# Performance work log

Hardware: AMD Instinct MI355X
Metric: run time of the kernel (lower is better)

The kernel has to match this reference:

```python
import jax, jax.numpy as jnp
import numpy as np

B, N, C, H = 4, 1024, 768, 12
HD = C // H

def setup_inputs() -> dict:
    key = jax.random.key(0)
    ks = jax.random.split(key, 6)
    s = 0.02
    return {
        "x": jax.random.normal(ks[0], (B, N, C), jnp.float32),
        "attn_bias": jax.random.normal(ks[1], (H, N, N), jnp.float32),
        "qkv_w": jax.random.normal(ks[2], (C, 3 * C), jnp.float32) * s,
        "qkv_b": jax.random.normal(ks[3], (3 * C,), jnp.float32) * s,
        "proj_w": jax.random.normal(ks[4], (C, C), jnp.float32) * s,
        "proj_b": jax.random.normal(ks[5], (C,), jnp.float32) * s,
    }

def reference(x, attn_bias, qkv_w, qkv_b, proj_w, proj_b):
    b, n, c = x.shape
    scale = HD ** -0.5
    qkv = x @ qkv_w + qkv_b                      # [B,N,3C]
    qkv = qkv.reshape(b, n, 3, H, HD)
    q = qkv[:, :, 0].transpose(0, 2, 1, 3)       # [B,H,N,HD]
    k = qkv[:, :, 1].transpose(0, 2, 1, 3)
    v = qkv[:, :, 2].transpose(0, 2, 1, 3)
    attn = jnp.einsum('bhqd,bhkd->bhqk', q, k) * scale
    attn = attn + attn_bias[None]                # broadcast over batch
    attn = jax.nn.softmax(attn, axis=-1)
    y = jnp.einsum('bhqk,bhkd->bhqd', attn, v)   # [B,H,N,HD]
    y = y.transpose(0, 2, 1, 3).reshape(b, n, c)
    return y @ proj_w + proj_b
```

## Files before the change

### kernel.cpp

```cpp
#include <hip/hip_runtime.h>
#include <hip/hip_bf16.h>

constexpr int BATCH = 4;
constexpr int NSEQ  = 1024;
constexpr int CDIM  = 768;
constexpr int NHEAD = 12;
constexpr int HDIM  = 64;
constexpr int MTOT  = BATCH * NSEQ;
constexpr int QKVN  = 3 * CDIM;

typedef __bf16 bf16x8 __attribute__((ext_vector_type(8)));
typedef float  f32x4  __attribute__((ext_vector_type(4)));

__device__ __forceinline__ unsigned short f2bf(float f) {
    unsigned u = __builtin_bit_cast(unsigned, f);
    unsigned r = u + 0x7FFFu + ((u >> 16) & 1u);
    return (unsigned short)(r >> 16);
}

#define GLOAD_LDS16(gp, lp)                                                    \
    __builtin_amdgcn_global_load_lds(                                          \
        (const __attribute__((address_space(1))) void*)(gp),                   \
        (__attribute__((address_space(3))) void*)(lp), 16, 0, 0)

__global__ __launch_bounds__(256) void cvt_f32_bf16(
    const float* __restrict__ in, unsigned short* __restrict__ out, int n4)
{
    int i = blockIdx.x * 256 + threadIdx.x;
    if (i < n4) {
        float4 a = reinterpret_cast<const float4*>(in)[i];
        ushort4 h;
        h.x = f2bf(a.x); h.y = f2bf(a.y); h.z = f2bf(a.z); h.w = f2bf(a.w);
        reinterpret_cast<ushort4*>(out)[i] = h;
    }
}

__global__ __launch_bounds__(256) void tcvt_f32_bf16(
    const float* __restrict__ in, unsigned short* __restrict__ out, int R, int C)
{
    __shared__ unsigned short t[32][33];
    const int c0 = blockIdx.x * 32, r0 = blockIdx.y * 32;
    const int tc = threadIdx.x & 31, tr = threadIdx.x >> 5;
    #pragma unroll
    for (int i = 0; i < 4; i++)
        t[tc][tr + 8 * i] = f2bf(in[(size_t)(r0 + tr + 8 * i) * C + c0 + tc]);
    __syncthreads();
    #pragma unroll
    for (int i = 0; i < 4; i++)
        out[(size_t)(c0 + tr + 8 * i) * R + r0 + tc] = t[tr + 8 * i][tc];
}

__global__ __launch_bounds__(256) void qkv_gemm(
    const unsigned short* __restrict__ xb,
    const unsigned short* __restrict__ wt,
    const float* __restrict__ bias,
    unsigned short* __restrict__ qbuf, unsigned short* __restrict__ kbuf,
    unsigned short* __restrict__ vtbuf)
{
    __shared__ unsigned short As[128 * 32];
    __shared__ unsigned short Bs[128 * 32];
    const int tid  = threadIdx.x;
    const int lane = tid & 63;
    const int wid  = tid >> 6;
    const int wm = (wid >> 1) * 64, wn = (wid & 1) * 64;
    const int g = lane >> 4, li = lane & 15;
    const int m0 = blockIdx.y * 128;
    const int n0 = blockIdx.x * 128;
    const int srow = lane >> 2;
    const int scol = (lane & 3) * 8;

    f32x4 acc[4][4];
    #pragma unroll
    for (int i = 0; i < 4; i++)
        #pragma unroll
        for (int j = 0; j < 4; j++) acc[i][j] = f32x4{0.f, 0.f, 0.f, 0.f};

    for (int k0 = 0; k0 < CDIM; k0 += 32) {
        __syncthreads();
        #pragma unroll
        for (int c = 0; c < 2; c++) {
            int row = wid * 32 + c * 16 + srow;
            GLOAD_LDS16(&xb[(size_t)(m0 + row) * CDIM + k0 + scol],
                        &As[(wid * 32 + c * 16) * 32]);
            GLOAD_LDS16(&wt[(size_t)(n0 + row) * CDIM + k0 + scol],
                        &Bs[(wid * 32 + c * 16) * 32]);
        }
        __syncthreads();
        bf16x8 a[4], b[4];
        #pragma unroll
        for (int mt = 0; mt < 4; mt++)
            a[mt] = *reinterpret_cast<const bf16x8*>(&As[(wm + 16 * mt + li) * 32 + 8 * g]);
        #pragma unroll
        for (int nt = 0; nt < 4; nt++)
            b[nt] = *reinterpret_cast<const bf16x8*>(&Bs[(wn + 16 * nt + li) * 32 + 8 * g]);
        #pragma unroll
        for (int mt = 0; mt < 4; mt++)
            #pragma unroll
            for (int nt = 0; nt < 4; nt++)
                acc[mt][nt] = __builtin_amdgcn_mfma_f32_16x16x32_bf16(a[mt], b[nt], acc[mt][nt], 0, 0, 0);
    }

    #pragma unroll
    for (int mt = 0; mt < 4; mt++) {
        #pragma unroll
        for (int nt = 0; nt < 4; nt++) {
            int col  = n0 + wn + 16 * nt + li;
            int tsel = col / CDIM;
            int rem  = col - tsel * CDIM;
            int h_ = rem >> 6, d = rem & 63;
            float bv = bias[col];
            float sc = (tsel == 0) ? 0.125f : 1.0f;
            #pragma unroll
            for (int r = 0; r < 4; r++) {
                int m  = m0 + wm + 16 * mt + 4 * g + r;
                int b_ = m >> 10, s = m & 1023;
                unsigned short hv = f2bf((acc[mt][nt][r] + bv) * sc);
                if (tsel == 0)
                    qbuf[(((size_t)b_ * NHEAD + h_) * NSEQ + s) * HDIM + d] = hv;
                else if (tsel == 1)
                    kbuf[(((size_t)b_ * NHEAD + h_) * NSEQ + s) * HDIM + d] = hv;
                else
                    vtbuf[(((size_t)b_ * NHEAD + h_) * HDIM + d) * NSEQ + s] = hv;
            }
        }
    }
}

__global__ __launch_bounds__(256, 3) void attn_kernel(
    const unsigned short* __restrict__ qbuf,
    const unsigned short* __restrict__ kbuf,
    const unsigned short* __restrict__ vtbuf,
    const float* __restrict__ bias,
    unsigned short* __restrict__ ybuf)
{
    __shared__ unsigned short Kl[2][64 * 64];
    __shared__ unsigned short Vl[2][64 * 64];
    __shared__ unsigned short Ps[4][16][72];

    const int tid  = threadIdx.x;
    const int lane = tid & 63;
    const int wid  = tid >> 6;
    const int g = lane >> 4, li = lane & 15;
    const int srow8 = lane >> 3;
    const int scs   = (lane & 7) ^ srow8;
    const int bh = blockIdx.y;
    const int b_ = bh / NHEAD, h_ = bh % NHEAD;
    const int qw = blockIdx.x * 64 + wid * 16;

    const unsigned short* qb = qbuf + (size_t)bh * NSEQ * HDIM;
    const unsigned short* kb = kbuf + (size_t)bh * NSEQ * HDIM;
    const unsigned short* vb = vtbuf + (size_t)bh * HDIM * NSEQ;
    const float* bb = bias + (size_t)h_ * NSEQ * NSEQ;

#define STAGE_KV(T, KL, VL)                                                    \
    {                                                                          \
        _Pragma("unroll") for (int i = 0; i < 2; i++) {                        \
            GLOAD_LDS16(kb + (size_t)((T) * 64 + wid * 16 + i * 8 + srow8) * HDIM + scs * 8, \
                        (KL) + (wid * 16 + i * 8) * 64);                       \
            GLOAD_LDS16(vb + (size_t)(wid * 16 + i * 8 + srow8) * NSEQ + (T) * 64 + scs * 8, \
                        (VL) + (wid * 16 + i * 8) * 64);                       \
        }                                                                      \
    }

#define COMPUTE_TILE(KS, VS, T)                                                \
    {                                                                          \
        float bv[4][4];                                                        \
        _Pragma("unroll") for (int kt = 0; kt < 4; kt++)                       \
            _Pragma("unroll") for (int r = 0; r < 4; r++)                      \
                bv[kt][r] = bb[(size_t)(qw + 4 * g + r) * NSEQ + (T) * 64 + 16 * kt + li]; \
        f32x4 sacc[4];                                                         \
        _Pragma("unroll") for (int kt = 0; kt < 4; kt++)                       \
            sacc[kt] = f32x4{0.f, 0.f, 0.f, 0.f};                              \
        _Pragma("unroll") for (int kt = 0; kt < 4; kt++)                       \
            _Pragma("unroll") for (int dd = 0; dd < 2; dd++) {                 \
                bf16x8 kf = *reinterpret_cast<const bf16x8*>(                  \
                    (KS) + (16 * kt + li) * 64 + (((4 * dd + g) ^ (li & 7)) * 8)); \
                sacc[kt] = __builtin_amdgcn_mfma_f32_16x16x32_bf16(qf[dd], kf, sacc[kt], 0, 0, 0); \
            }                                                                  \
        _Pragma("unroll") for (int kt = 0; kt < 4; kt++)                       \
            _Pragma("unroll") for (int r = 0; r < 4; r++) {                    \
                float pv = __expf(sacc[kt][r] + bv[kt][r]);                    \
                lpart[r] += pv;                                                \
                Ps[wid][4 * g + r][16 * kt + li] = f2bf(pv);                   \
            }                                                                  \
        _Pragma("unroll") for (int kk = 0; kk < 2; kk++) {                     \
            bf16x8 pf = *reinterpret_cast<const bf16x8*>(&Ps[wid][li][32 * kk + 8 * g]); \
            _Pragma("unroll") for (int dt = 0; dt < 4; dt++) {                 \
                bf16x8 vf = *reinterpret_cast<const bf16x8*>(                  \
                    (VS) + (16 * dt + li) * 64 + (((4 * kk + g) ^ (li & 7)) * 8)); \
                oacc[dt] = __builtin_amdgcn_mfma_f32_16x16x32_bf16(pf, vf, oacc[dt], 0, 0, 0); \
            }                                                                  \
        }                                                                      \
    }

    bf16x8 qf[2];
    #pragma unroll
    for (int dd = 0; dd < 2; dd++)
        qf[dd] = *reinterpret_cast<const bf16x8*>(&qb[(size_t)(qw + li) * HDIM + 32 * dd + 8 * g]);

    f32x4 oacc[4];
    #pragma unroll
    for (int dt = 0; dt < 4; dt++) oacc[dt] = f32x4{0.f, 0.f, 0.f, 0.f};
    float lpart[4] = {0.f, 0.f, 0.f, 0.f};

    STAGE_KV(0, Kl[0], Vl[0]);
    __syncthreads();

    for (int j = 0; j < 8; ++j) {
        const int tA = 2 * j;
        STAGE_KV(tA + 1, Kl[1], Vl[1]);
        COMPUTE_TILE(Kl[0], Vl[0], tA);
        __syncthreads();

        if (j < 7) STAGE_KV(tA + 2, Kl[0], Vl[0]);
        COMPUTE_TILE(Kl[1], Vl[1], tA + 1);
        __syncthreads();
    }

    float linv[4];
    #pragma unroll
    for (int r = 0; r < 4; r++) {
        float s = lpart[r];
        s += __shfl_xor(s, 1);
        s += __shfl_xor(s, 2);
        s += __shfl_xor(s, 4);
        s += __shfl_xor(s, 8);
        linv[r] = 1.f / s;
    }
    #pragma unroll
    for (int dt = 0; dt < 4; dt++)
        #pragma unroll
        for (int r = 0; r < 4; r++) {
            float o = oacc[dt][r] * linv[r];
            int sq = qw + 4 * g + r;
            ybuf[((size_t)b_ * NSEQ + sq) * CDIM + h_ * HDIM + 16 * dt + li] = f2bf(o);
        }
#undef STAGE_KV
#undef COMPUTE_TILE
}

__global__ __launch_bounds__(256) void proj_gemm(
    const unsigned short* __restrict__ yb,
    const unsigned short* __restrict__ pwt,
    const float* __restrict__ bias, float* __restrict__ out)
{
    __shared__ unsigned short As[128 * 32];
    __shared__ unsigned short Bs[128 * 32];
    const int tid  = threadIdx.x;
    const int lane = tid & 63;
    const int wid  = tid >> 6;
    const int wm = (wid >> 1) * 64, wn = (wid & 1) * 64;
    const int g = lane >> 4, li = lane & 15;
    const int m0 = blockIdx.y * 128;
    const int n0 = blockIdx.x * 128;
    const int srow = lane >> 2;
    const int scol = (lane & 3) * 8;

    f32x4 acc[4][4];
    #pragma unroll
    for (int i = 0; i < 4; i++)
        #pragma unroll
        for (int j = 0; j < 4; j++) acc[i][j] = f32x4{0.f, 0.f, 0.f, 0.f};

    for (int k0 = 0; k0 < CDIM; k0 += 32) {
        __syncthreads();
        #pragma unroll
        for (int c = 0; c < 2; c++) {
            int row = wid * 32 + c * 16 + srow;
            GLOAD_LDS16(&yb[(size_t)(m0 + row) * CDIM + k0 + scol],
                        &As[(wid * 32 + c * 16) * 32]);
            GLOAD_LDS16(&pwt[(size_t)(n0 + row) * CDIM + k0 + scol],
                        &Bs[(wid * 32 + c * 16) * 32]);
        }
        __syncthreads();
        bf16x8 a[4], b[4];
        #pragma unroll
        for (int mt = 0; mt < 4; mt++)
            a[mt] = *reinterpret_cast<const bf16x8*>(&As[(wm + 16 * mt + li) * 32 + 8 * g]);
        #pragma unroll
        for (int nt = 0; nt < 4; nt++)
            b[nt] = *reinterpret_cast<const bf16x8*>(&Bs[(wn + 16 * nt + li) * 32 + 8 * g]);
        #pragma unroll
        for (int mt = 0; mt < 4; mt++)
            #pragma unroll
            for (int nt = 0; nt < 4; nt++)
                acc[mt][nt] = __builtin_amdgcn_mfma_f32_16x16x32_bf16(a[mt], b[nt], acc[mt][nt], 0, 0, 0);
    }

    #pragma unroll
    for (int mt = 0; mt < 4; mt++)
        #pragma unroll
        for (int nt = 0; nt < 4; nt++) {
            int col = n0 + wn + 16 * nt + li;
            float bv = bias[col];
            #pragma unroll
            for (int r = 0; r < 4; r++) {
                int m = m0 + wm + 16 * mt + 4 * g + r;
                out[(size_t)m * CDIM + col] = acc[mt][nt][r] + bv;
            }
        }
}

extern "C" void kernel_launch(void* const* d_in, const int* in_sizes, int n_in,
                              void* d_out, int out_size, void* d_ws, size_t ws_size,
                              hipStream_t stream) {
    const float* x         = (const float*)d_in[0];
    const float* attn_bias = (const float*)d_in[1];
    const float* qkv_w     = (const float*)d_in[2];
    const float* qkv_b     = (const float*)d_in[3];
    const float* proj_w    = (const float*)d_in[4];
    const float* proj_b    = (const float*)d_in[5];
    float* out = (float*)d_out;

    const size_t per = (size_t)BATCH * NHEAD * NSEQ * HDIM;
    unsigned short* qbuf  = (unsigned short*)d_ws;
    unsigned short* kbuf  = qbuf + per;
    unsigned short* vtbuf = kbuf + per;
    unsigned short* xb    = vtbuf + per;
    unsigned short* qwt   = xb + per;
    unsigned short* pwt   = qwt + (size_t)QKVN * CDIM;
    unsigned short* ybuf  = xb;

    cvt_f32_bf16<<<(MTOT * CDIM / 4 + 255) / 256, 256, 0, stream>>>(
        x, xb, MTOT * CDIM / 4);
    tcvt_f32_bf16<<<dim3(QKVN / 32, CDIM / 32), 256, 0, stream>>>(
        qkv_w, qwt, CDIM, QKVN);
    tcvt_f32_bf16<<<dim3(CDIM / 32, CDIM / 32), 256, 0, stream>>>(
        proj_w, pwt, CDIM, CDIM);

    qkv_gemm<<<dim3(QKVN / 128, MTOT / 128), 256, 0, stream>>>(
        xb, qwt, qkv_b, qbuf, kbuf, vtbuf);
    attn_kernel<<<dim3(NSEQ / 64, BATCH * NHEAD), 256, 0, stream>>>(
        qbuf, kbuf, vtbuf, attn_bias, ybuf);
    proj_gemm<<<dim3(CDIM / 128, MTOT / 128), 256, 0, stream>>>(
        ybuf, pwt, proj_b, out);
}
```

Before: 106.8 us.

## Split attention over key halves, keep P in registers, add combine kernel

The attention kernel now splits the 1024 keys into two halves across a third grid dimension, writing unnormalised bf16 partial outputs and row sums that a new combine kernel merges and normalises. Scores are computed as K·Q so that exponentiated probabilities can be packed directly into MFMA operand registers, removing the LDS staging of P. The QKV GEMM permutes K rows within 32-row groups to match this layout, and the bias is loaded with vector loads. This raises block count and occupancy, at the cost of an extra kernel launch, extra workspace traffic, and a bf16 rounding of partial outputs.

Result: slower. 121.5 us (+13.7%).

```diff
diff --git a/kernel.cpp b/kernel.cpp
--- a/kernel.cpp
+++ b/kernel.cpp
@@ -8,6 +8,7 @@
 constexpr int HDIM  = 64;
 constexpr int MTOT  = BATCH * NSEQ;
 constexpr int QKVN  = 3 * CDIM;
+constexpr int NBH   = BATCH * NHEAD;
 
 typedef __bf16 bf16x8 __attribute__((ext_vector_type(8)));
 typedef float  f32x4  __attribute__((ext_vector_type(4)));
@@ -16,6 +17,13 @@
     unsigned u = __builtin_bit_cast(unsigned, f);
     unsigned r = u + 0x7FFFu + ((u >> 16) & 1u);
     return (unsigned short)(r >> 16);
+}
+__device__ __forceinline__ float bf2f(unsigned short h) {
+    unsigned u = ((unsigned)h) << 16;
+    return __builtin_bit_cast(float, u);
+}
+__device__ __forceinline__ unsigned pack_bf16(float lo, float hi) {
+    return (unsigned)f2bf(lo) | ((unsigned)f2bf(hi) << 16);
 }
 
 #define GLOAD_LDS16(gp, lp)                                                    \
@@ -117,77 +125,94 @@
                 unsigned short hv = f2bf((acc[mt][nt][r] + bv) * sc);
                 if (tsel == 0)
                     qbuf[(((size_t)b_ * NHEAD + h_) * NSEQ + s) * HDIM + d] = hv;
-                else if (tsel == 1)
-                    kbuf[(((size_t)b_ * NHEAD + h_) * NSEQ + s) * HDIM + d] = hv;
-                else
+                else if (tsel == 1) {
+                    int sp = (s & 0x3E3) | ((s & 4) << 2) | ((s & 0x18) >> 1);
+                    kbuf[(((size_t)b_ * NHEAD + h_) * NSEQ + sp) * HDIM + d] = hv;
+                } else
                     vtbuf[(((size_t)b_ * NHEAD + h_) * HDIM + d) * NSEQ + s] = hv;
             }
         }
     }
 }
 
-__global__ __launch_bounds__(256, 3) void attn_kernel(
+__global__ __launch_bounds__(256, 5) void attn_kernel(
     const unsigned short* __restrict__ qbuf,
     const unsigned short* __restrict__ kbuf,
     const unsigned short* __restrict__ vtbuf,
     const float* __restrict__ bias,
-    unsigned short* __restrict__ ybuf)
+    unsigned short* __restrict__ osplit,
+    float* __restrict__ lsplit)
 {
     __shared__ unsigned short Kl[2][64 * 64];
     __shared__ unsigned short Vl[2][64 * 64];
-    __shared__ unsigned short Ps[4][16][72];
 
     const int tid  = threadIdx.x;
     const int lane = tid & 63;
     const int wid  = tid >> 6;
     const int g = lane >> 4, li = lane & 15;
     const int srow8 = lane >> 3;
-    const int scs   = (lane & 7) ^ srow8;
+    const int scs8  = (lane & 7) ^ srow8;
     const int bh = blockIdx.y;
     const int b_ = bh / NHEAD, h_ = bh % NHEAD;
     const int qw = blockIdx.x * 64 + wid * 16;
+    const int z  = blockIdx.z;
+    const int t0 = z * 8;
 
     const unsigned short* qb = qbuf + (size_t)bh * NSEQ * HDIM;
     const unsigned short* kb = kbuf + (size_t)bh * NSEQ * HDIM;
     const unsigned short* vb = vtbuf + (size_t)bh * HDIM * NSEQ;
     const float* bb = bias + (size_t)h_ * NSEQ * NSEQ;
-
-#define STAGE_KV(T, KL, VL)                                                    \
+    unsigned short* osz = osplit + (size_t)z * NBH * NSEQ * HDIM;
+    float* lsz = lsplit + (size_t)z * NBH * NSEQ;
+
+#define STAGE(T, KL, VL)                                                       \
     {                                                                          \
         _Pragma("unroll") for (int i = 0; i < 2; i++) {                        \
-            GLOAD_LDS16(kb + (size_t)((T) * 64 + wid * 16 + i * 8 + srow8) * HDIM + scs * 8, \
+            GLOAD_LDS16(kb + (size_t)((T) * 64 + wid * 16 + i * 8 + srow8) * HDIM + scs8 * 8, \
                         (KL) + (wid * 16 + i * 8) * 64);                       \
-            GLOAD_LDS16(vb + (size_t)(wid * 16 + i * 8 + srow8) * NSEQ + (T) * 64 + scs * 8, \
+            GLOAD_LDS16(vb + (size_t)(wid * 16 + i * 8 + srow8) * NSEQ + (T) * 64 + scs8 * 8, \
                         (VL) + (wid * 16 + i * 8) * 64);                       \
         }                                                                      \
     }
 
-#define COMPUTE_TILE(KS, VS, T)                                                \
+#define COMPUTE(KS, VS, K0)                                                    \
     {                                                                          \
-        float bv[4][4];                                                        \
-        _Pragma("unroll") for (int kt = 0; kt < 4; kt++)                       \
-            _Pragma("unroll") for (int r = 0; r < 4; r++)                      \
-                bv[kt][r] = bb[(size_t)(qw + 4 * g + r) * NSEQ + (T) * 64 + 16 * kt + li]; \
-        f32x4 sacc[4];                                                         \
-        _Pragma("unroll") for (int kt = 0; kt < 4; kt++)                       \
-            sacc[kt] = f32x4{0.f, 0.f, 0.f, 0.f};                              \
-        _Pragma("unroll") for (int kt = 0; kt < 4; kt++)                       \
+        const float* bp = &bb[(size_t)(qw + li) * NSEQ + (K0) + 8 * g];        \
+        f32x4 b00 = *reinterpret_cast<const f32x4*>(bp);                       \
+        f32x4 b01 = *reinterpret_cast<const f32x4*>(bp + 4);                   \
+        f32x4 b10 = *reinterpret_cast<const f32x4*>(bp + 32);                  \
+        f32x4 b11 = *reinterpret_cast<const f32x4*>(bp + 36);                  \
+        _Pragma("unroll") for (int sl = 0; sl < 2; sl++) {                     \
+            f32x4 s0 = f32x4{0.f, 0.f, 0.f, 0.f};                              \
+            f32x4 s1 = f32x4{0.f, 0.f, 0.f, 0.f};                              \
             _Pragma("unroll") for (int dd = 0; dd < 2; dd++) {                 \
-                bf16x8 kf = *reinterpret_cast<const bf16x8*>(                  \
-                    (KS) + (16 * kt + li) * 64 + (((4 * dd + g) ^ (li & 7)) * 8)); \
-                sacc[kt] = __builtin_amdgcn_mfma_f32_16x16x32_bf16(qf[dd], kf, sacc[kt], 0, 0, 0); \
+                bf16x8 kf0 = *reinterpret_cast<const bf16x8*>(                 \
+                    (KS) + (32 * sl + li) * 64 + (((4 * dd + g) ^ (li & 7)) * 8)); \
+                bf16x8 kf1 = *reinterpret_cast<const bf16x8*>(                 \
+                    (KS) + (32 * sl + 16 + li) * 64 + (((4 * dd + g) ^ (li & 7)) * 8)); \
+                s0 = __builtin_amdgcn_mfma_f32_16x16x32_bf16(kf0, qf[dd], s0, 0, 0, 0); \
+                s1 = __builtin_amdgcn_mfma_f32_16x16x32_bf16(kf1, qf[dd], s1, 0, 0, 0); \
             }                                                                  \
-        _Pragma("unroll") for (int kt = 0; kt < 4; kt++)                       \
-            _Pragma("unroll") for (int r = 0; r < 4; r++) {                    \
-                float pv = __expf(sacc[kt][r] + bv[kt][r]);                    \
-                lpart[r] += pv;                                                \
-                Ps[wid][4 * g + r][16 * kt + li] = f2bf(pv);                   \
-            }                                                                  \
-        _Pragma("unroll") for (int kk = 0; kk < 2; kk++) {                     \
-            bf16x8 pf = *reinterpret_cast<const bf16x8*>(&Ps[wid][li][32 * kk + 8 * g]); \
+            f32x4 blo = sl ? b10 : b00;                                        \
+            f32x4 bhi = sl ? b11 : b01;                                        \
+            float p0 = __expf(s0[0] + blo[0]);                                 \
+            float p1 = __expf(s0[1] + blo[1]);                                 \
+            float p2 = __expf(s0[2] + blo[2]);                                 \
+            float p3 = __expf(s0[3] + blo[3]);                                 \
+            float p4 = __expf(s1[0] + bhi[0]);                                 \
+            float p5 = __expf(s1[1] + bhi[1]);                                 \
+            float p6 = __expf(s1[2] + bhi[2]);                                 \
+            float p7 = __expf(s1[3] + bhi[3]);                                 \
+            lpart += ((p0 + p1) + (p2 + p3)) + ((p4 + p5) + (p6 + p7));        \
+            uint4 pw;                                                          \
+            pw.x = pack_bf16(p0, p1);                                          \
+            pw.y = pack_bf16(p2, p3);                                          \
+            pw.z = pack_bf16(p4, p5);                                          \
+            pw.w = pack_bf16(p6, p7);                                          \
+            bf16x8 pf = __builtin_bit_cast(bf16x8, pw);                        \
             _Pragma("unroll") for (int dt = 0; dt < 4; dt++) {                 \
                 bf16x8 vf = *reinterpret_cast<const bf16x8*>(                  \
-                    (VS) + (16 * dt + li) * 64 + (((4 * kk + g) ^ (li & 7)) * 8)); \
+                    (VS) + (16 * dt + li) * 64 + (((4 * sl + g) ^ (li & 7)) * 8)); \
                 oacc[dt] = __builtin_amdgcn_mfma_f32_16x16x32_bf16(pf, vf, oacc[dt], 0, 0, 0); \
             }                                                                  \
         }                                                                      \
@@ -201,42 +226,62 @@
     f32x4 oacc[4];
     #pragma unroll
     for (int dt = 0; dt < 4; dt++) oacc[dt] = f32x4{0.f, 0.f, 0.f, 0.f};
-    float lpart[4] = {0.f, 0.f, 0.f, 0.f};
-
-    STAGE_KV(0, Kl[0], Vl[0]);
+    float lpart = 0.f;
+
+    STAGE(t0, Kl[0], Vl[0]);
     __syncthreads();
 
-    for (int j = 0; j < 8; ++j) {
-        const int tA = 2 * j;
-        STAGE_KV(tA + 1, Kl[1], Vl[1]);
-        COMPUTE_TILE(Kl[0], Vl[0], tA);
-        __syncthreads();
-
-        if (j < 7) STAGE_KV(tA + 2, Kl[0], Vl[0]);
-        COMPUTE_TILE(Kl[1], Vl[1], tA + 1);
-        __syncthreads();
-    }
-
-    float linv[4];
-    #pragma unroll
-    for (int r = 0; r < 4; r++) {
-        float s = lpart[r];
-        s += __shfl_xor(s, 1);
-        s += __shfl_xor(s, 2);
-        s += __shfl_xor(s, 4);
-        s += __shfl_xor(s, 8);
-        linv[r] = 1.f / s;
-    }
+    for (int j = 0; j < 4; ++j) {
+        const int tA = t0 + 2 * j;
+        STAGE(tA + 1, Kl[1], Vl[1]);
+        COMPUTE(Kl[0], Vl[0], tA * 64);
+        __syncthreads();
+        if (j < 3) STAGE(tA + 2, Kl[0], Vl[0]);
+        COMPUTE(Kl[1], Vl[1], (tA + 1) * 64);
+        __syncthreads();
+    }
+
+    lpart += __shfl_xor(lpart, 16);
+    lpart += __shfl_xor(lpart, 32);
+    if (lane < 16)
+        lsz[(size_t)bh * NSEQ + qw + lane] = lpart;
+
     #pragma unroll
     for (int dt = 0; dt < 4; dt++)
         #pragma unroll
         for (int r = 0; r < 4; r++) {
-            float o = oacc[dt][r] * linv[r];
             int sq = qw + 4 * g + r;
-            ybuf[((size_t)b_ * NSEQ + sq) * CDIM + h_ * HDIM + 16 * dt + li] = f2bf(o);
-        }
-#undef STAGE_KV
-#undef COMPUTE_TILE
+            osz[((size_t)bh * NSEQ + sq) * HDIM + 16 * dt + li] = f2bf(oacc[dt][r]);
+        }
+#undef STAGE
+#undef COMPUTE
+}
+
+__global__ __launch_bounds__(256) void combine_kernel(
+    const unsigned short* __restrict__ osplit,
+    const float* __restrict__ lsplit,
+    unsigned short* __restrict__ ybuf)
+{
+    const int tid = threadIdx.x;
+    const int row = blockIdx.x * 16 + (tid >> 4);
+    const int d0  = (tid & 15) * 4;
+    const size_t HALF_O = (size_t)NBH * NSEQ * HDIM;
+    const size_t HALF_L = (size_t)NBH * NSEQ;
+
+    float l = lsplit[row] + lsplit[HALF_L + row];
+    float inv = 1.f / l;
+    ushort4 a = *reinterpret_cast<const ushort4*>(&osplit[(size_t)row * HDIM + d0]);
+    ushort4 b = *reinterpret_cast<const ushort4*>(&osplit[HALF_O + (size_t)row * HDIM + d0]);
+    ushort4 o;
+    o.x = f2bf((bf2f(a.x) + bf2f(b.x)) * inv);
+    o.y = f2bf((bf2f(a.y) + bf2f(b.y)) * inv);
+    o.z = f2bf((bf2f(a.z) + bf2f(b.z)) * inv);
+    o.w = f2bf((bf2f(a.w) + bf2f(b.w)) * inv);
+
+    int bh = row >> 10, q = row & 1023;
+    int b_ = bh / NHEAD, h_ = bh % NHEAD;
+    *reinterpret_cast<ushort4*>(
+        &ybuf[((size_t)b_ * NSEQ + q) * CDIM + h_ * HDIM + d0]) = o;
 }
 
 __global__ __launch_bounds__(256) void proj_gemm(
@@ -312,13 +357,15 @@
     const float* proj_b    = (const float*)d_in[5];
     float* out = (float*)d_out;
 
-    const size_t per = (size_t)BATCH * NHEAD * NSEQ * HDIM;
+    const size_t per = (size_t)NBH * NSEQ * HDIM;
     unsigned short* qbuf  = (unsigned short*)d_ws;
     unsigned short* kbuf  = qbuf + per;
     unsigned short* vtbuf = kbuf + per;
     unsigned short* xb    = vtbuf + per;
     unsigned short* qwt   = xb + per;
     unsigned short* pwt   = qwt + (size_t)QKVN * CDIM;
+    unsigned short* osplit = pwt + (size_t)CDIM * CDIM;
+    float* lsplit = (float*)(osplit + 2 * per);
     unsigned short* ybuf  = xb;
 
     cvt_f32_bf16<<<(MTOT * CDIM / 4 + 255) / 256, 256, 0, stream>>>(
@@ -330,8 +377,10 @@
 
     qkv_gemm<<<dim3(QKVN / 128, MTOT / 128), 256, 0, stream>>>(
         xb, qwt, qkv_b, qbuf, kbuf, vtbuf);
-    attn_kernel<<<dim3(NSEQ / 64, BATCH * NHEAD), 256, 0, stream>>>(
-        qbuf, kbuf, vtbuf, attn_bias, ybuf);
+    attn_kernel<<<dim3(NSEQ / 64, NBH, 2), 256, 0, stream>>>(
+        qbuf, kbuf, vtbuf, attn_bias, osplit, lsplit);
+    combine_kernel<<<NBH * NSEQ / 16, 256, 0, stream>>>(
+        osplit, lsplit, ybuf);
     proj_gemm<<<dim3(CDIM / 128, MTOT / 128), 256, 0, stream>>>(
         ybuf, pwt, proj_b, out);
 }
```

## Double-buffer LDS in QKV and projection GEMMs and halve M tile to 64

Applied to the files above, without the earlier changes.

Both GEMM kernels now use two LDS buffers with a ping-pong loop, so the next K slice is loaded while MFMAs run on the current one, and one barrier is removed per step. The M tile shrinks from 128 to 64 rows, which doubles the grid (proj goes from 192 to 384 blocks) to improve CU fill on a 256-CU part. Each block does less reuse per loaded B tile, so global and L2 traffic for the weights increases.

After: 106.0 us. No clear change (-0.8%).

```diff
diff --git a/kernel.cpp b/kernel.cpp
--- a/kernel.cpp
+++ b/kernel.cpp
@@ -57,54 +57,66 @@
     unsigned short* __restrict__ qbuf, unsigned short* __restrict__ kbuf,
     unsigned short* __restrict__ vtbuf)
 {
-    __shared__ unsigned short As[128 * 32];
-    __shared__ unsigned short Bs[128 * 32];
+    __shared__ unsigned short A0[64 * 32], A1[64 * 32];
+    __shared__ unsigned short B0[128 * 32], B1[128 * 32];
     const int tid  = threadIdx.x;
     const int lane = tid & 63;
     const int wid  = tid >> 6;
-    const int wm = (wid >> 1) * 64, wn = (wid & 1) * 64;
+    const int wr = (wid >> 1) * 32, wc = (wid & 1) * 64;
     const int g = lane >> 4, li = lane & 15;
-    const int m0 = blockIdx.y * 128;
+    const int m0 = blockIdx.y * 64;
     const int n0 = blockIdx.x * 128;
     const int srow = lane >> 2;
     const int scol = (lane & 3) * 8;
 
-    f32x4 acc[4][4];
-    #pragma unroll
-    for (int i = 0; i < 4; i++)
+#define QSTAGE(K0, AD, BD)                                                     \
+    {                                                                          \
+        GLOAD_LDS16(&xb[(size_t)(m0 + wid * 16 + srow) * CDIM + (K0) + scol],  \
+                    (AD) + wid * 16 * 32);                                     \
+        _Pragma("unroll") for (int c = 0; c < 2; c++)                          \
+            GLOAD_LDS16(&wt[(size_t)(n0 + wid * 32 + c * 16 + srow) * CDIM + (K0) + scol], \
+                        (BD) + (wid * 32 + c * 16) * 32);                      \
+    }
+
+#define QCOMPUTE(AS, BS)                                                       \
+    {                                                                          \
+        bf16x8 a[2], b[4];                                                     \
+        _Pragma("unroll") for (int mt = 0; mt < 2; mt++)                       \
+            a[mt] = *reinterpret_cast<const bf16x8*>(                          \
+                (AS) + (wr + 16 * mt + li) * 32 + 8 * g);                      \
+        _Pragma("unroll") for (int nt = 0; nt < 4; nt++)                       \
+            b[nt] = *reinterpret_cast<const bf16x8*>(                          \
+                (BS) + (wc + 16 * nt + li) * 32 + 8 * g);                      \
+        _Pragma("unroll") for (int mt = 0; mt < 2; mt++)                       \
+            _Pragma("unroll") for (int nt = 0; nt < 4; nt++)                   \
+                acc[mt][nt] = __builtin_amdgcn_mfma_f32_16x16x32_bf16(         \
+                    a[mt], b[nt], acc[mt][nt], 0, 0, 0);                       \
+    }
+
+    f32x4 acc[2][4];
+    #pragma unroll
+    for (int i = 0; i < 2; i++)
         #pragma unroll
         for (int j = 0; j < 4; j++) acc[i][j] = f32x4{0.f, 0.f, 0.f, 0.f};
 
-    for (int k0 = 0; k0 < CDIM; k0 += 32) {
-        __syncthreads();
-        #pragma unroll
-        for (int c = 0; c < 2; c++) {
-            int row = wid * 32 + c * 16 + srow;
-            GLOAD_LDS16(&xb[(size_t)(m0 + row) * CDIM + k0 + scol],
-                        &As[(wid * 32 + c * 16) * 32]);
-            GLOAD_LDS16(&wt[(size_t)(n0 + row) * CDIM + k0 + scol],
-                        &Bs[(wid * 32 + c * 16) * 32]);
-        }
-        __syncthreads();
-        bf16x8 a[4], b[4];
-        #pragma unroll
-        for (int mt = 0; mt < 4; mt++)
-            a[mt] = *reinterpret_cast<const bf16x8*>(&As[(wm + 16 * mt + li) * 32 + 8 * g]);
-        #pragma unroll
-        for (int nt = 0; nt < 4; nt++)
-            b[nt] = *reinterpret_cast<const bf16x8*>(&Bs[(wn + 16 * nt + li) * 32 + 8 * g]);
-        #pragma unroll
-        for (int mt = 0; mt < 4; mt++)
-            #pragma unroll
-            for (int nt = 0; nt < 4; nt++)
-                acc[mt][nt] = __builtin_amdgcn_mfma_f32_16x16x32_bf16(a[mt], b[nt], acc[mt][nt], 0, 0, 0);
-    }
-
-    #pragma unroll
-    for (int mt = 0; mt < 4; mt++) {
+    QSTAGE(0, A0, B0);
+    __syncthreads();
+
+    for (int j = 0; j < 12; ++j) {
+        const int k0 = j * 64;
+        QSTAGE(k0 + 32, A1, B1);
+        QCOMPUTE(A0, B0);
+        __syncthreads();
+        if (j < 11) QSTAGE(k0 + 64, A0, B0);
+        QCOMPUTE(A1, B1);
+        __syncthreads();
+    }
+
+    #pragma unroll
+    for (int mt = 0; mt < 2; mt++) {
         #pragma unroll
         for (int nt = 0; nt < 4; nt++) {
-            int col  = n0 + wn + 16 * nt + li;
+            int col  = n0 + wc + 16 * nt + li;
             int tsel = col / CDIM;
             int rem  = col - tsel * CDIM;
             int h_ = rem >> 6, d = rem & 63;
@@ -112,7 +124,7 @@
             float sc = (tsel == 0) ? 0.125f : 1.0f;
             #pragma unroll
             for (int r = 0; r < 4; r++) {
-                int m  = m0 + wm + 16 * mt + 4 * g + r;
+                int m  = m0 + wr + 16 * mt + 4 * g + r;
                 int b_ = m >> 10, s = m & 1023;
                 unsigned short hv = f2bf((acc[mt][nt][r] + bv) * sc);
                 if (tsel == 0)
@@ -124,6 +136,8 @@
             }
         }
     }
+#undef QSTAGE
+#undef QCOMPUTE
 }
 
 __global__ __launch_bounds__(256, 3) void attn_kernel(
@@ -244,61 +258,75 @@
     const unsigned short* __restrict__ pwt,
     const float* __restrict__ bias, float* __restrict__ out)
 {
-    __shared__ unsigned short As[128 * 32];
-    __shared__ unsigned short Bs[128 * 32];
+    __shared__ unsigned short A0[64 * 32], A1[64 * 32];
+    __shared__ unsigned short B0[128 * 32], B1[128 * 32];
     const int tid  = threadIdx.x;
     const int lane = tid & 63;
     const int wid  = tid >> 6;
-    const int wm = (wid >> 1) * 64, wn = (wid & 1) * 64;
+    const int wr = (wid >> 1) * 32, wc = (wid & 1) * 64;
     const int g = lane >> 4, li = lane & 15;
-    const int m0 = blockIdx.y * 128;
+    const int m0 = blockIdx.y * 64;
     const int n0 = blockIdx.x * 128;
     const int srow = lane >> 2;
     const int scol = (lane & 3) * 8;
 
-    f32x4 acc[4][4];
-    #pragma unroll
-    for (int i = 0; i < 4; i++)
+#define PSTAGE(K0, AD, BD)                                                     \
+    {                                                                          \
+        GLOAD_LDS16(&yb[(size_t)(m0 + wid * 16 + srow) * CDIM + (K0) + scol],  \
+                    (AD) + wid * 16 * 32);                                     \
+        _Pragma("unroll") for (int c = 0; c < 2; c++)                          \
+            GLOAD_LDS16(&pwt[(size_t)(n0 + wid * 32 + c * 16 + srow) * CDIM + (K0) + scol], \
+                        (BD) + (wid * 32 + c * 16) * 32);                      \
+    }
+
+#define PCOMPUTE(AS, BS)                                                       \
+    {                                                                          \
+        bf16x8 a[2], b[4];                                                     \
+        _Pragma("unroll") for (int mt = 0; mt < 2; mt++)                       \
+            a[mt] = *reinterpret_cast<const bf16x8*>(                          \
+                (AS) + (wr + 16 * mt + li) * 32 + 8 * g);                      \
+        _Pragma("unroll") for (int nt = 0; nt < 4; nt++)                       \
+            b[nt] = *reinterpret_cast<const bf16x8*>(                          \
+                (BS) + (wc + 16 * nt + li) * 32 + 8 * g);                      \
+        _Pragma("unroll") for (int mt = 0; mt < 2; mt++)                       \
+            _Pragma("unroll") for (int nt = 0; nt < 4; nt++)                   \
+                acc[mt][nt] = __builtin_amdgcn_mfma_f32_16x16x32_bf16(         \
+                    a[mt], b[nt], acc[mt][nt], 0, 0, 0);                       \
+    }
+
+    f32x4 acc[2][4];
+    #pragma unroll
+    for (int i = 0; i < 2; i++)
         #pragma unroll
         for (int j = 0; j < 4; j++) acc[i][j] = f32x4{0.f, 0.f, 0.f, 0.f};
 
-    for (int k0 = 0; k0 < CDIM; k0 += 32) {
-        __syncthreads();
-        #pragma unroll
-        for (int c = 0; c < 2; c++) {
-            int row = wid * 32 + c * 16 + srow;
-            GLOAD_LDS16(&yb[(size_t)(m0 + row) * CDIM + k0 + scol],
-                        &As[(wid * 32 + c * 16) * 32]);
-            GLOAD_LDS16(&pwt[(size_t)(n0 + row) * CDIM + k0 + scol],
-                        &Bs[(wid * 32 + c * 16) * 32]);
-        }
-        __syncthreads();
-        bf16x8 a[4], b[4];
-        #pragma unroll
-        for (int mt = 0; mt < 4; mt++)
-            a[mt] = *reinterpret_cast<const bf16x8*>(&As[(wm + 16 * mt + li) * 32 + 8 * g]);
-        #pragma unroll
-        for (int nt = 0; nt < 4; nt++)
-            b[nt] = *reinterpret_cast<const bf16x8*>(&Bs[(wn + 16 * nt + li) * 32 + 8 * g]);
-        #pragma unroll
-        for (int mt = 0; mt < 4; mt++)
-            #pragma unroll
-            for (int nt = 0; nt < 4; nt++)
-                acc[mt][nt] = __builtin_amdgcn_mfma_f32_16x16x32_bf16(a[mt], b[nt], acc[mt][nt], 0, 0, 0);
-    }
-
-    #pragma unroll
-    for (int mt = 0; mt < 4; mt++)
+    PSTAGE(0, A0, B0);
+    __syncthreads();
+
+    for (int j = 0; j < 12; ++j) {
+        const int k0 = j * 64;
+        PSTAGE(k0 + 32, A1, B1);
+        PCOMPUTE(A0, B0);
+        __syncthreads();
+        if (j < 11) PSTAGE(k0 + 64, A0, B0);
+        PCOMPUTE(A1, B1);
+        __syncthreads();
+    }
+
+    #pragma unroll
+    for (int mt = 0; mt < 2; mt++)
         #pragma unroll
         for (int nt = 0; nt < 4; nt++) {
-            int col = n0 + wn + 16 * nt + li;
+            int col = n0 + wc + 16 * nt + li;
             float bv = bias[col];
             #pragma unroll
             for (int r = 0; r < 4; r++) {
-                int m = m0 + wm + 16 * mt + 4 * g + r;
+                int m = m0 + wr + 16 * mt + 4 * g + r;
                 out[(size_t)m * CDIM + col] = acc[mt][nt][r] + bv;
             }
         }
+#undef PSTAGE
+#undef PCOMPUTE
 }
 
 extern "C" void kernel_launch(void* const* d_in, const int* in_sizes, int n_in,
@@ -328,10 +356,10 @@
     tcvt_f32_bf16<<<dim3(CDIM / 32, CDIM / 32), 256, 0, stream>>>(
         proj_w, pwt, CDIM, CDIM);
 
-    qkv_gemm<<<dim3(QKVN / 128, MTOT / 128), 256, 0, stream>>>(
+    qkv_gemm<<<dim3(QKVN / 128, MTOT / 64), 256, 0, stream>>>(
         xb, qwt, qkv_b, qbuf, kbuf, vtbuf);
     attn_kernel<<<dim3(NSEQ / 64, BATCH * NHEAD), 256, 0, stream>>>(
         qbuf, kbuf, vtbuf, attn_bias, ybuf);
-    proj_gemm<<<dim3(CDIM / 128, MTOT / 128), 256, 0, stream>>>(
+    proj_gemm<<<dim3(CDIM / 128, MTOT / 64), 256, 0, stream>>>(
         ybuf, pwt, proj_b, out);
 }
```
